# Optimization experiments

Measured on AMD Instinct MI355X. Metric: run time of the kernel, lower is better.

Reference implementation:

```python
import jax, jax.numpy as jnp
import numpy as np

BS, N, H = 8, 64, 512
L = 5
HH, WW = 14, 14


def setup_inputs() -> dict:
    key = jax.random.key(0)
    ks = jax.random.split(key, 6)
    roi_feature_single = jax.random.normal(ks[0], (BS, N, H), dtype=jnp.float32)
    img_featmap = jax.random.normal(ks[1], (BS, H, HH, WW), dtype=jnp.float32)
    # torch init: weight ~ N(0, 0.01), bias = 0
    node_W = jax.random.normal(ks[2], (L, H, H), dtype=jnp.float32) * 0.01
    node_b = jnp.zeros((L, H), dtype=jnp.float32)
    edge_W = jax.random.normal(ks[3], (L, H, H), dtype=jnp.float32) * 0.01
    edge_b = jnp.zeros((L, H), dtype=jnp.float32)
    full_mask = jax.random.randint(ks[4], (BS, N, N), 0, 2, dtype=jnp.int32)
    return {
        "roi_feature_single": roi_feature_single,
        "img_featmap": img_featmap,
        "node_W": node_W,
        "node_b": node_b,
        "edge_W": edge_W,
        "edge_b": edge_b,
        "full_mask": full_mask,
    }


def reference(roi_feature_single, img_featmap, node_W, node_b, edge_W, edge_b, full_mask):
    # mask: [bs, N, N, 1], float
    mask = full_mask.astype(jnp.float32)[..., None]
    denom = jnp.sum(mask, axis=-2) + 1.0  # [bs, N, 1]

    # AdaptiveAvgPool2d((1,1)) on N*N repeats of img_featmap == global mean over (H, W)
    edge_init = jnp.mean(img_featmap, axis=(2, 3))  # [bs, hidden]
    edge_state = jnp.broadcast_to(edge_init[:, None, None, :], (BS, N, N, H))

    node_state = roi_feature_single  # [bs, N, hidden]

    for t in range(L):
        nm = jnp.einsum('bnh,oh->bno', node_state, node_W[t]) + node_b[t]          # node_fc
        em = jnp.einsum('bijh,oh->bijo', edge_state, edge_W[t]) + edge_b[t]        # edge_fc
        col = nm[:, None, :, :]                      # feature_col_large [bs,1,N,h]
        edge_feat = nm[:, :, None, :] + col + em     # row + col + edge messages
        edge_state = jax.nn.leaky_relu(edge_feat)    # negative_slope=0.01 (torch default)
        agg = jnp.sum(edge_state * col * mask, axis=-2)   # masked sum over j -> [bs,N,h]
        node_feat = (nm + agg) / denom
        node_state = node_state + jax.nn.leaky_relu(node_feat)

    roi_col = jnp.broadcast_to(node_state[:, :, None, :], (BS, N, N, H))
    roi_row = jnp.broadcast_to(node_state[:, None, :, :], (BS, N, N, H))
    return jnp.concatenate([roi_col, roi_row], axis=-1)  # [bs, N, N, 2*hidden]
```

## Files before the change

### kernel.cpp

```cpp
#include <hip/hip_runtime.h>
#include <hip/hip_bf16.h>

#define BS 8
#define NN 64
#define HD 512
#define NLAYER 5

typedef short bf16x8 __attribute__((ext_vector_type(8)));
typedef float f32x4 __attribute__((ext_vector_type(4)));

__device__ __forceinline__ float lrelu(float x) { return x > 0.f ? x : 0.01f * x; }

__device__ __forceinline__ void cp16(const void* g, void* l) {
    __builtin_amdgcn_global_load_lds(
        (const __attribute__((address_space(1))) unsigned int*)g,
        (__attribute__((address_space(3))) unsigned int*)l,
        16, 0, 0);
}

__global__ __launch_bounds__(256) void prep_kernel(
    const float* __restrict__ roi, const float* __restrict__ img,
    const float* __restrict__ nW, const float* __restrict__ eW,
    const int* __restrict__ mask,
    __hip_bfloat16* __restrict__ nWb, __hip_bfloat16* __restrict__ eWb,
    float* __restrict__ nodef, __hip_bfloat16* __restrict__ nodeb,
    float* __restrict__ edge_init, float* __restrict__ denom)
{
    int bid = blockIdx.x, tid = threadIdx.x;
    if (bid < 2560) {
        const float* src = (bid < 1280) ? nW : eW;
        __hip_bfloat16* dst = (bid < 1280) ? nWb : eWb;
        int base = ((bid < 1280) ? bid : bid - 1280) * 1024 + tid * 4;
#pragma unroll
        for (int k = 0; k < 4; ++k) dst[base + k] = __float2bfloat16(src[base + k]);
    } else if (bid < 2816) {
        int base = (bid - 2560) * 1024 + tid * 4;
#pragma unroll
        for (int k = 0; k < 4; ++k) {
            float v = roi[base + k];
            nodef[base + k] = v;
            nodeb[base + k] = __float2bfloat16(v);
        }
    } else if (bid < 3840) {
        int pid = (bid - 2816) * 4 + (tid >> 6);
        int l = tid & 63;
        const float* p = img + (size_t)pid * 196;
        float s = 0.f;
        for (int x = l; x < 196; x += 64) s += p[x];
#pragma unroll
        for (int off = 1; off < 64; off <<= 1) s += __shfl_xor(s, off, 64);
        if (l == 0) edge_init[pid] = s * (1.f / 196.f);
    } else {
        int pid = (bid - 3840) * 256 + tid;
        if (pid < 512) {
            const int* m = mask + pid * 64;
            int s = 0;
#pragma unroll
            for (int j = 0; j < 64; ++j) s += m[j];
            denom[pid] = (float)s + 1.f;
        }
    }
}

__global__ __launch_bounds__(256) void em0_kernel(
    const float* __restrict__ edge_init,
    const float* __restrict__ eW0,
    const float* __restrict__ eB0,
    float* __restrict__ em0)
{
    int W = blockIdx.x * 4 + (threadIdx.x >> 6);
    int l = threadIdx.x & 63;
    int b = W >> 9, o = W & 511;
    const float4* ei = (const float4*)(edge_init + b * 512);
    const float4* w4 = (const float4*)(eW0 + (size_t)o * 512);
    float4 a0 = ei[l * 2], a1 = ei[l * 2 + 1];
    float4 b0 = w4[l * 2], b1 = w4[l * 2 + 1];
    float s = a0.x * b0.x + a0.y * b0.y + a0.z * b0.z + a0.w * b0.w
            + a1.x * b1.x + a1.y * b1.y + a1.z * b1.z + a1.w * b1.w;
#pragma unroll
    for (int off = 1; off < 64; off <<= 1) s += __shfl_xor(s, off, 64);
    if (l == 0) em0[W] = s + eB0[o];
}

__global__ __launch_bounds__(256) void nm_gemm(
    const __hip_bfloat16* __restrict__ A,
    const __hip_bfloat16* __restrict__ W,
    const float* __restrict__ bias,
    float* __restrict__ nm)
{
    __shared__ __align__(16) __hip_bfloat16 sA[64 * 32];
    __shared__ __align__(16) __hip_bfloat16 sB[64 * 32];
    int tid = threadIdx.x;
    int bm = blockIdx.x, bn = blockIdx.y;
    int w = tid >> 6, l = tid & 63;
    int lq = l >> 4, lr = l & 15;

    const char* aBase = (const char*)A + (size_t)bm * 64 * 1024;
    const char* bBase = (const char*)W + (size_t)bn * 64 * 1024;
    int r2 = tid >> 2;
    int offG = r2 * 1024 + ((((tid & 3) ^ (r2 & 3))) << 4);
    int offL = tid * 16;
    int sw = lr & 3;

    f32x4 acc[4] = {};

    for (int kt = 0; kt < 16; ++kt) {
        int ko = kt * 64;
        cp16(aBase + offG + ko, (char*)sA + offL);
        cp16(bBase + offG + ko, (char*)sB + offL);
        __syncthreads();
        bf16x8 af = *(const bf16x8*)&sA[(w * 16 + lr) * 32 + ((lq ^ sw) << 3)];
#pragma unroll
        for (int ni = 0; ni < 4; ++ni) {
            bf16x8 bfv = *(const bf16x8*)&sB[(ni * 16 + lr) * 32 + ((lq ^ sw) << 3)];
            acc[ni] = __builtin_amdgcn_mfma_f32_16x16x32_bf16(af, bfv, acc[ni], 0, 0, 0);
        }
        __syncthreads();
    }
#pragma unroll
    for (int ni = 0; ni < 4; ++ni) {
        int col = bn * 64 + ni * 16 + lr;
        float bv = bias[col];
#pragma unroll
        for (int r = 0; r < 4; ++r) {
            int row = bm * 64 + w * 16 + lq * 4 + r;
            nm[(size_t)row * 512 + col] = acc[ni][r] + bv;
        }
    }
}

__global__ __launch_bounds__(256) void edge_rank1(
    const float* __restrict__ nm, const float* __restrict__ em0,
    const int* __restrict__ mask,
    __hip_bfloat16* __restrict__ es_dst,
    const float* __restrict__ denom,
    float* __restrict__ nodef, __hip_bfloat16* __restrict__ nodeb)
{
    int g = blockIdx.x >> 1, ch = blockIdx.x & 1;
    int w = threadIdx.x >> 6, l = threadIdx.x & 63;
    int c = ch * 256 + w * 64 + l;
    int b = g >> 6;
    float nmi = nm[(size_t)g * 512 + c];
    float emb = em0[b * 512 + c];
    const float* nmb = nm + (size_t)b * 64 * 512;
    const int* mrow = mask + g * 64;
    __hip_bfloat16* erow = es_dst + (size_t)g * 64 * 512 + c;
    float aggv = 0.f;
#pragma unroll 4
    for (int j = 0; j < 64; ++j) {
        float nmj = nmb[j * 512 + c];
        float es = lrelu(nmi + nmj + emb);
        erow[(size_t)j * 512] = __float2bfloat16(es);
        aggv += es * nmj * (float)mrow[j];
    }
    float nf = (nmi + aggv) / denom[g];
    size_t idx = (size_t)g * 512 + c;
    float ns = nodef[idx] + lrelu(nf);
    nodef[idx] = ns;
    nodeb[idx] = __float2bfloat16(ns);
}

__global__ __launch_bounds__(256) void edge_fused(
    const __hip_bfloat16* __restrict__ es_src,
    const __hip_bfloat16* __restrict__ eW,
    const float* __restrict__ eB,
    const float* __restrict__ nm,
    const int* __restrict__ mask,
    __hip_bfloat16* __restrict__ es_dst,
    const float* __restrict__ denom,
    float* __restrict__ nodef, __hip_bfloat16* __restrict__ nodeb,
    int write_es)
{
    __shared__ __align__(16) __hip_bfloat16 sA[128 * 64];
    __shared__ __align__(16) __hip_bfloat16 sB[128 * 64];
    int tid = threadIdx.x;
    int lid = blockIdx.y * 4 + blockIdx.x;
    int xcd = lid & 7, idx = lid >> 3;
    int bm = xcd + ((idx >> 2) << 3);
    int bn = idx & 3;
    int w = tid >> 6, l = tid & 63;
    int wm = w >> 1, wn = w & 1;
    int lq = l >> 4, lr = l & 15;

    const char* aBase = (const char*)es_src + (size_t)bm * 128 * 1024;
    const char* bBase = (const char*)eW + (size_t)bn * 128 * 1024;
    int rrow = tid >> 3;
    int gOff = rrow * 1024 + ((((tid & 7) ^ (rrow & 7))) << 4);
    int lOff = tid * 16;
    int sw = lr & 7;

    f32x4 acc[4][4] = {};

    for (int kt = 0; kt < 8; ++kt) {
        int ko = kt * 128;
#pragma unroll
        for (int i = 0; i < 4; ++i) {
            cp16(aBase + gOff + i * 32768 + ko, (char*)sA + lOff + i * 4096);
            cp16(bBase + gOff + i * 32768 + ko, (char*)sB + lOff + i * 4096);
        }
        __syncthreads();
#pragma unroll
        for (int kk = 0; kk < 2; ++kk) {
            bf16x8 af[4], bfv[4];
#pragma unroll
            for (int mi = 0; mi < 4; ++mi)
                af[mi] = *(const bf16x8*)&sA[(wm * 64 + mi * 16 + lr) * 64 + (((kk * 4 + lq) ^ sw) << 3)];
#pragma unroll
            for (int ni = 0; ni < 4; ++ni)
                bfv[ni] = *(const bf16x8*)&sB[(wn * 64 + ni * 16 + lr) * 64 + (((kk * 4 + lq) ^ sw) << 3)];
#pragma unroll
            for (int mi = 0; mi < 4; ++mi)
#pragma unroll
                for (int ni = 0; ni < 4; ++ni)
                    acc[mi][ni] = __builtin_amdgcn_mfma_f32_16x16x32_bf16(af[mi], bfv[ni], acc[mi][ni], 0, 0, 0);
        }
        __syncthreads();
    }

    int g = bm * 2 + wm;
    int b = g >> 6;
    int cbase = bn * 128 + wn * 64;

    float nmraw[4], nmi[4];
#pragma unroll
    for (int ni = 0; ni < 4; ++ni) {
        int c = cbase + ni * 16 + lr;
        nmraw[ni] = nm[(size_t)g * 512 + c];
        nmi[ni] = nmraw[ni] + eB[c];
    }
    const float* nmb = nm + (size_t)b * 64 * 512;
    const int* mrow = mask + g * 64;
    float aggv[4] = {0.f, 0.f, 0.f, 0.f};

#pragma unroll
    for (int mi = 0; mi < 4; ++mi) {
#pragma unroll
        for (int r = 0; r < 4; ++r) {
            int j = mi * 16 + lq * 4 + r;
            float mf = (float)mrow[j];
            const float* nrow = nmb + (size_t)j * 512;
            size_t erow = ((size_t)(g * 64 + j)) * 512;
#pragma unroll
            for (int ni = 0; ni < 4; ++ni) {
                int c = cbase + ni * 16 + lr;
                float nmj = nrow[c];
                float es = lrelu(acc[mi][ni][r] + nmi[ni] + nmj);
                if (write_es) es_dst[erow + c] = __float2bfloat16(es);
                aggv[ni] += es * nmj * mf;
            }
        }
    }
    float dinv = denom[g];
#pragma unroll
    for (int ni = 0; ni < 4; ++ni) {
        float v = aggv[ni];
        v += __shfl_xor(v, 16, 64);
        v += __shfl_xor(v, 32, 64);
        if (lq == 0) {
            size_t idx = (size_t)g * 512 + cbase + ni * 16 + lr;
            float nf = (nmraw[ni] + v) / dinv;
            float ns = nodef[idx] + lrelu(nf);
            nodef[idx] = ns;
            nodeb[idx] = __float2bfloat16(ns);
        }
    }
}

__global__ __launch_bounds__(256) void out_kernel(
    const float* __restrict__ nodef, float* __restrict__ out)
{
    size_t ch = (size_t)blockIdx.x * 256 + threadIdx.x;
    int c4 = (int)(ch & 255);
    size_t r = ch >> 8;
    int b = (int)(r >> 12);
    int i = (int)((r >> 6) & 63);
    int j = (int)(r & 63);
    int c = c4 * 4;
    const float* src = (c < 512) ? (nodef + ((size_t)(b * 64 + i)) * 512 + c)
                                 : (nodef + ((size_t)(b * 64 + j)) * 512 + (c - 512));
    *reinterpret_cast<float4*>(out + ch * 4) = *reinterpret_cast<const float4*>(src);
}

extern "C" void kernel_launch(void* const* d_in, const int* in_sizes, int n_in,
                              void* d_out, int out_size, void* d_ws, size_t ws_size,
                              hipStream_t stream) {
    const float* roi  = (const float*)d_in[0];
    const float* img  = (const float*)d_in[1];
    const float* nW   = (const float*)d_in[2];
    const float* nB   = (const float*)d_in[3];
    const float* eW   = (const float*)d_in[4];
    const float* eB   = (const float*)d_in[5];
    const int*   mask = (const int*)d_in[6];

    char* ob = (char*)d_out;
    const size_t ES_BYTES = (size_t)32768 * 512 * 2;
    __hip_bfloat16* es0   = (__hip_bfloat16*)(ob);
    __hip_bfloat16* es1   = (__hip_bfloat16*)(ob + ES_BYTES);
    __hip_bfloat16* eWb   = (__hip_bfloat16*)(ob + 2 * ES_BYTES);
    __hip_bfloat16* nWb   = (__hip_bfloat16*)(ob + 2 * ES_BYTES + 2621440);
    __hip_bfloat16* nodeb = (__hip_bfloat16*)(ob + 2 * ES_BYTES + 5242880);
    float*          nm    = (float*)(ob + 2 * ES_BYTES + 5767168);
    float*       edge_init= (float*)(ob + 2 * ES_BYTES + 6815744);
    float*          em0   = (float*)(ob + 2 * ES_BYTES + 6832128);

    char* ws = (char*)d_ws;
    float* nodef = (float*)(ws);
    float* denom = (float*)(ws + 1048576);
    float* outp  = (float*)d_out;

    prep_kernel<<<3842, 256, 0, stream>>>(roi, img, nW, eW, mask,
                                          nWb, eWb, nodef, nodeb, edge_init, denom);
    em0_kernel<<<1024, 256, 0, stream>>>(edge_init, eW, eB, em0);

    nm_gemm<<<dim3(8, 8), 256, 0, stream>>>(nodeb, nWb, nB, nm);
    edge_rank1<<<1024, 256, 0, stream>>>(nm, em0, mask, es0, denom, nodef, nodeb);

    for (int t = 1; t < NLAYER; ++t) {
        const __hip_bfloat16* src = (t & 1) ? es0 : es1;
        __hip_bfloat16* dst       = (t & 1) ? es1 : es0;
        nm_gemm<<<dim3(8, 8), 256, 0, stream>>>(nodeb, nWb + (size_t)t * 262144,
                                                nB + t * 512, nm);
        edge_fused<<<dim3(4, 256), 256, 0, stream>>>(src, eWb + (size_t)t * 262144,
                                                     eB + t * 512, nm, mask,
                                                     dst, denom, nodef, nodeb,
                                                     (t < 4) ? 1 : 0);
    }

    out_kernel<<<32768, 256, 0, stream>>>(nodef, outp);
}
```

Measured before the change: 430.8 us.

## Double-buffer LDS tiles in node and edge GEMMs to overlap loads with MFMA

```diff
diff --git a/kernel.cpp b/kernel.cpp
--- a/kernel.cpp
+++ b/kernel.cpp
@@ -88,8 +88,8 @@
     const float* __restrict__ bias,
     float* __restrict__ nm)
 {
-    __shared__ __align__(16) __hip_bfloat16 sA[64 * 32];
-    __shared__ __align__(16) __hip_bfloat16 sB[64 * 32];
+    __shared__ __align__(16) __hip_bfloat16 sA[2][64 * 32];
+    __shared__ __align__(16) __hip_bfloat16 sB[2][64 * 32];
     int tid = threadIdx.x;
     int bm = blockIdx.x, bn = blockIdx.y;
     int w = tid >> 6, l = tid & 63;
@@ -104,19 +104,35 @@
 
     f32x4 acc[4] = {};
 
-    for (int kt = 0; kt < 16; ++kt) {
-        int ko = kt * 64;
-        cp16(aBase + offG + ko, (char*)sA + offL);
-        cp16(bBase + offG + ko, (char*)sB + offL);
+#define NM_STAGE(kt, bsel) do { \
+        int ko = (kt) * 64; \
+        cp16(aBase + offG + ko, (char*)sA[bsel] + offL); \
+        cp16(bBase + offG + ko, (char*)sB[bsel] + offL); \
+    } while (0)
+
+#define NM_COMPUTE(bsel) do { \
+        bf16x8 af = *(const bf16x8*)&sA[bsel][(w * 16 + lr) * 32 + ((lq ^ sw) << 3)]; \
+        bf16x8 bfv[4]; \
+        _Pragma("unroll") \
+        for (int ni = 0; ni < 4; ++ni) \
+            bfv[ni] = *(const bf16x8*)&sB[bsel][(ni * 16 + lr) * 32 + ((lq ^ sw) << 3)]; \
+        __builtin_amdgcn_s_setprio(1); \
+        _Pragma("unroll") \
+        for (int ni = 0; ni < 4; ++ni) \
+            acc[ni] = __builtin_amdgcn_mfma_f32_16x16x32_bf16(af, bfv[ni], acc[ni], 0, 0, 0); \
+        __builtin_amdgcn_s_setprio(0); \
+    } while (0)
+
+    NM_STAGE(0, 0);
+    __syncthreads();
+#pragma unroll 2
+    for (int kt = 0; kt < 15; ++kt) {
+        NM_STAGE(kt + 1, (kt & 1) ^ 1);
+        NM_COMPUTE(kt & 1);
         __syncthreads();
-        bf16x8 af = *(const bf16x8*)&sA[(w * 16 + lr) * 32 + ((lq ^ sw) << 3)];
-#pragma unroll
-        for (int ni = 0; ni < 4; ++ni) {
-            bf16x8 bfv = *(const bf16x8*)&sB[(ni * 16 + lr) * 32 + ((lq ^ sw) << 3)];
-            acc[ni] = __builtin_amdgcn_mfma_f32_16x16x32_bf16(af, bfv, acc[ni], 0, 0, 0);
-        }
-        __syncthreads();
-    }
+    }
+    NM_COMPUTE(1);
+
 #pragma unroll
     for (int ni = 0; ni < 4; ++ni) {
         int col = bn * 64 + ni * 16 + lr;
@@ -127,6 +143,8 @@
             nm[(size_t)row * 512 + col] = acc[ni][r] + bv;
         }
     }
+#undef NM_STAGE
+#undef NM_COMPUTE
 }
 
 __global__ __launch_bounds__(256) void edge_rank1(
@@ -171,8 +189,8 @@
     float* __restrict__ nodef, __hip_bfloat16* __restrict__ nodeb,
     int write_es)
 {
-    __shared__ __align__(16) __hip_bfloat16 sA[128 * 64];
-    __shared__ __align__(16) __hip_bfloat16 sB[128 * 64];
+    __shared__ __align__(16) __hip_bfloat16 sA[2][128 * 32];
+    __shared__ __align__(16) __hip_bfloat16 sB[2][128 * 32];
     int tid = threadIdx.x;
     int lid = blockIdx.y * 4 + blockIdx.x;
     int xcd = lid & 7, idx = lid >> 3;
@@ -184,43 +202,50 @@
 
     const char* aBase = (const char*)es_src + (size_t)bm * 128 * 1024;
     const char* bBase = (const char*)eW + (size_t)bn * 128 * 1024;
-    int rrow = tid >> 3;
-    int gOff = rrow * 1024 + ((((tid & 7) ^ (rrow & 7))) << 4);
-    int lOff = tid * 16;
-    int sw = lr & 7;
+    int r0 = tid >> 2, c16 = tid & 3;
+    int g0 = r0 * 1024 + (((c16 ^ (r0 & 3))) << 4);
+    int l0 = tid * 16;
+    int swr = lr & 3;
 
     f32x4 acc[4][4] = {};
 
-    for (int kt = 0; kt < 8; ++kt) {
-        int ko = kt * 128;
-#pragma unroll
-        for (int i = 0; i < 4; ++i) {
-            cp16(aBase + gOff + i * 32768 + ko, (char*)sA + lOff + i * 4096);
-            cp16(bBase + gOff + i * 32768 + ko, (char*)sB + lOff + i * 4096);
-        }
-        __syncthreads();
-#pragma unroll
-        for (int kk = 0; kk < 2; ++kk) {
-            bf16x8 af[4], bfv[4];
-#pragma unroll
-            for (int mi = 0; mi < 4; ++mi)
-                af[mi] = *(const bf16x8*)&sA[(wm * 64 + mi * 16 + lr) * 64 + (((kk * 4 + lq) ^ sw) << 3)];
-#pragma unroll
-            for (int ni = 0; ni < 4; ++ni)
-                bfv[ni] = *(const bf16x8*)&sB[(wn * 64 + ni * 16 + lr) * 64 + (((kk * 4 + lq) ^ sw) << 3)];
-#pragma unroll
-            for (int mi = 0; mi < 4; ++mi)
-#pragma unroll
-                for (int ni = 0; ni < 4; ++ni)
-                    acc[mi][ni] = __builtin_amdgcn_mfma_f32_16x16x32_bf16(af[mi], bfv[ni], acc[mi][ni], 0, 0, 0);
-        }
+#define EF_STAGE(kt, bsel) do { \
+        int ko = (kt) * 64; \
+        cp16(aBase + g0 + ko,         (char*)sA[bsel] + l0); \
+        cp16(aBase + g0 + 65536 + ko, (char*)sA[bsel] + l0 + 4096); \
+        cp16(bBase + g0 + ko,         (char*)sB[bsel] + l0); \
+        cp16(bBase + g0 + 65536 + ko, (char*)sB[bsel] + l0 + 4096); \
+    } while (0)
+
+#define EF_COMPUTE(bsel) do { \
+        bf16x8 af[4], bfv[4]; \
+        _Pragma("unroll") \
+        for (int mi = 0; mi < 4; ++mi) \
+            af[mi] = *(const bf16x8*)&sA[bsel][(wm * 64 + mi * 16 + lr) * 32 + ((lq ^ swr) << 3)]; \
+        _Pragma("unroll") \
+        for (int ni = 0; ni < 4; ++ni) \
+            bfv[ni] = *(const bf16x8*)&sB[bsel][(wn * 64 + ni * 16 + lr) * 32 + ((lq ^ swr) << 3)]; \
+        __builtin_amdgcn_s_setprio(1); \
+        _Pragma("unroll") \
+        for (int mi = 0; mi < 4; ++mi) \
+            _Pragma("unroll") \
+            for (int ni = 0; ni < 4; ++ni) \
+                acc[mi][ni] = __builtin_amdgcn_mfma_f32_16x16x32_bf16(af[mi], bfv[ni], acc[mi][ni], 0, 0, 0); \
+        __builtin_amdgcn_s_setprio(0); \
+    } while (0)
+
+    EF_STAGE(0, 0);
+    __syncthreads();
+#pragma unroll 2
+    for (int kt = 0; kt < 15; ++kt) {
+        EF_STAGE(kt + 1, (kt & 1) ^ 1);
+        EF_COMPUTE(kt & 1);
         __syncthreads();
     }
 
     int g = bm * 2 + wm;
     int b = g >> 6;
     int cbase = bn * 128 + wn * 64;
-
     float nmraw[4], nmi[4];
 #pragma unroll
     for (int ni = 0; ni < 4; ++ni) {
@@ -228,10 +253,13 @@
         nmraw[ni] = nm[(size_t)g * 512 + c];
         nmi[ni] = nmraw[ni] + eB[c];
     }
+    float dinv = denom[g];
     const float* nmb = nm + (size_t)b * 64 * 512;
     const int* mrow = mask + g * 64;
+
+    EF_COMPUTE(1);
+
     float aggv[4] = {0.f, 0.f, 0.f, 0.f};
-
 #pragma unroll
     for (int mi = 0; mi < 4; ++mi) {
 #pragma unroll
@@ -250,20 +278,21 @@
             }
         }
     }
-    float dinv = denom[g];
 #pragma unroll
     for (int ni = 0; ni < 4; ++ni) {
         float v = aggv[ni];
         v += __shfl_xor(v, 16, 64);
         v += __shfl_xor(v, 32, 64);
         if (lq == 0) {
-            size_t idx = (size_t)g * 512 + cbase + ni * 16 + lr;
+            size_t oidx = (size_t)g * 512 + cbase + ni * 16 + lr;
             float nf = (nmraw[ni] + v) / dinv;
-            float ns = nodef[idx] + lrelu(nf);
-            nodef[idx] = ns;
-            nodeb[idx] = __float2bfloat16(ns);
-        }
-    }
+            float ns = nodef[oidx] + lrelu(nf);
+            nodef[oidx] = ns;
+            nodeb[oidx] = __float2bfloat16(ns);
+        }
+    }
+#undef EF_STAGE
+#undef EF_COMPUTE
 }
 
 __global__ __launch_bounds__(256) void out_kernel(
```

Result: slower. 605.0 us (+40.4%).

## Retile node GEMM to 32x64 blocks with K=128 steps and add occupancy hints

Applied to the files above, without the earlier changes.

```diff
diff --git a/kernel.cpp b/kernel.cpp
--- a/kernel.cpp
+++ b/kernel.cpp
@@ -82,48 +82,53 @@
     if (l == 0) em0[W] = s + eB0[o];
 }
 
-__global__ __launch_bounds__(256) void nm_gemm(
+__global__ __launch_bounds__(256, 4) void nm_gemm(
     const __hip_bfloat16* __restrict__ A,
     const __hip_bfloat16* __restrict__ W,
     const float* __restrict__ bias,
     float* __restrict__ nm)
 {
-    __shared__ __align__(16) __hip_bfloat16 sA[64 * 32];
-    __shared__ __align__(16) __hip_bfloat16 sB[64 * 32];
+    __shared__ __align__(16) __hip_bfloat16 sA[32 * 64];
+    __shared__ __align__(16) __hip_bfloat16 sB[64 * 64];
     int tid = threadIdx.x;
     int bm = blockIdx.x, bn = blockIdx.y;
     int w = tid >> 6, l = tid & 63;
+    int wm = w & 1, wn = w >> 1;
     int lq = l >> 4, lr = l & 15;
 
-    const char* aBase = (const char*)A + (size_t)bm * 64 * 1024;
+    const char* aBase = (const char*)A + (size_t)bm * 32 * 1024;
     const char* bBase = (const char*)W + (size_t)bn * 64 * 1024;
-    int r2 = tid >> 2;
-    int offG = r2 * 1024 + ((((tid & 3) ^ (r2 & 3))) << 4);
-    int offL = tid * 16;
-    int sw = lr & 3;
-
-    f32x4 acc[4] = {};
-
-    for (int kt = 0; kt < 16; ++kt) {
-        int ko = kt * 64;
-        cp16(aBase + offG + ko, (char*)sA + offL);
-        cp16(bBase + offG + ko, (char*)sB + offL);
+    int rowA = tid >> 3;
+    int gA = rowA * 1024 + (((tid & 7) ^ (rowA & 7)) << 4);
+    int lO = tid * 16;
+    int sw = lr & 7;
+
+    f32x4 acc[2] = {};
+
+    for (int kt = 0; kt < 8; ++kt) {
+        int ko = kt * 128;
+        cp16(aBase + gA + ko, (char*)sA + lO);
+        cp16(bBase + gA + ko, (char*)sB + lO);
+        cp16(bBase + gA + 32768 + ko, (char*)sB + lO + 4096);
         __syncthreads();
-        bf16x8 af = *(const bf16x8*)&sA[(w * 16 + lr) * 32 + ((lq ^ sw) << 3)];
-#pragma unroll
-        for (int ni = 0; ni < 4; ++ni) {
-            bf16x8 bfv = *(const bf16x8*)&sB[(ni * 16 + lr) * 32 + ((lq ^ sw) << 3)];
-            acc[ni] = __builtin_amdgcn_mfma_f32_16x16x32_bf16(af, bfv, acc[ni], 0, 0, 0);
+#pragma unroll
+        for (int kk = 0; kk < 2; ++kk) {
+            bf16x8 af = *(const bf16x8*)&sA[(wm * 16 + lr) * 64 + (((kk * 4 + lq) ^ sw) << 3)];
+#pragma unroll
+            for (int ni = 0; ni < 2; ++ni) {
+                bf16x8 bv = *(const bf16x8*)&sB[(wn * 32 + ni * 16 + lr) * 64 + (((kk * 4 + lq) ^ sw) << 3)];
+                acc[ni] = __builtin_amdgcn_mfma_f32_16x16x32_bf16(af, bv, acc[ni], 0, 0, 0);
+            }
         }
         __syncthreads();
     }
 #pragma unroll
-    for (int ni = 0; ni < 4; ++ni) {
-        int col = bn * 64 + ni * 16 + lr;
+    for (int ni = 0; ni < 2; ++ni) {
+        int col = bn * 64 + wn * 32 + ni * 16 + lr;
         float bv = bias[col];
 #pragma unroll
         for (int r = 0; r < 4; ++r) {
-            int row = bm * 64 + w * 16 + lq * 4 + r;
+            int row = bm * 32 + wm * 16 + lq * 4 + r;
             nm[(size_t)row * 512 + col] = acc[ni][r] + bv;
         }
     }
@@ -160,7 +165,7 @@
     nodeb[idx] = __float2bfloat16(ns);
 }
 
-__global__ __launch_bounds__(256) void edge_fused(
+__global__ __launch_bounds__(256, 4) void edge_fused(
     const __hip_bfloat16* __restrict__ es_src,
     const __hip_bfloat16* __restrict__ eW,
     const float* __restrict__ eB,
@@ -257,11 +262,11 @@
         v += __shfl_xor(v, 16, 64);
         v += __shfl_xor(v, 32, 64);
         if (lq == 0) {
-            size_t idx = (size_t)g * 512 + cbase + ni * 16 + lr;
+            size_t oidx = (size_t)g * 512 + cbase + ni * 16 + lr;
             float nf = (nmraw[ni] + v) / dinv;
-            float ns = nodef[idx] + lrelu(nf);
-            nodef[idx] = ns;
-            nodeb[idx] = __float2bfloat16(ns);
+            float ns = nodef[oidx] + lrelu(nf);
+            nodef[oidx] = ns;
+            nodeb[oidx] = __float2bfloat16(ns);
         }
     }
 }
@@ -312,14 +317,14 @@
                                           nWb, eWb, nodef, nodeb, edge_init, denom);
     em0_kernel<<<1024, 256, 0, stream>>>(edge_init, eW, eB, em0);
 
-    nm_gemm<<<dim3(8, 8), 256, 0, stream>>>(nodeb, nWb, nB, nm);
+    nm_gemm<<<dim3(16, 8), 256, 0, stream>>>(nodeb, nWb, nB, nm);
     edge_rank1<<<1024, 256, 0, stream>>>(nm, em0, mask, es0, denom, nodef, nodeb);
 
     for (int t = 1; t < NLAYER; ++t) {
         const __hip_bfloat16* src = (t & 1) ? es0 : es1;
         __hip_bfloat16* dst       = (t & 1) ? es1 : es0;
-        nm_gemm<<<dim3(8, 8), 256, 0, stream>>>(nodeb, nWb + (size_t)t * 262144,
-                                                nB + t * 512, nm);
+        nm_gemm<<<dim3(16, 8), 256, 0, stream>>>(nodeb, nWb + (size_t)t * 262144,
+                                                 nB + t * 512, nm);
         edge_fused<<<dim3(4, 256), 256, 0, stream>>>(src, eWb + (size_t)t * 262144,
                                                      eB + t * 512, nm, mask,
                                                      dst, denom, nodef, nodeb,
```

Measured after the change: 400.8 us. 6.9% less time.
